# Performance work log

Measured on AMD Instinct MI355X. Metric: run time of the kernel, lower is better.

The kernel has to match this reference:

```python
import jax, jax.numpy as jnp
import numpy as np

N = 4096      # number of projected gaussians
W = 512       # screen width
H = 512       # screen height
TL = 64       # tile_length
NT = W // TL  # tiles per axis (8) -> NT*NT = 64 tiles


def setup_inputs() -> dict:
    key = jax.random.key(0)
    k1, k2, k3, k4, k5 = jax.random.split(key, 5)
    xy = jax.random.uniform(k1, (N, 2), dtype=jnp.float32) * W          # screen positions
    depth = jax.random.uniform(k2, (N, 1), dtype=jnp.float32) * 10.0 + 0.1
    pos2d = jnp.concatenate([xy, depth], axis=1)                        # [N,3] = (x, y, depth)
    A = jax.random.normal(k3, (N, 2, 2), dtype=jnp.float32)
    cov2d = 9.0 * jnp.einsum('nij,nkj->nik', A, A) + jnp.eye(2, dtype=jnp.float32)  # PSD, ~3px sigma
    opacity = jax.random.uniform(k4, (N,), dtype=jnp.float32)
    color = jax.random.uniform(k5, (N, 3), dtype=jnp.float32)           # SH-evaluated RGB (pre +0.5 clamp)
    return {"pos2d": pos2d, "cov2d": cov2d, "opacity": opacity, "color": color}


def _render(pos2d, cov2d, opacity, color):
    # Global depth sort == per-tile argsort of the masked subset (order is preserved).
    order = jnp.argsort(pos2d[:, 2])
    pos = pos2d[order]
    cov = cov2d[order]
    op = opacity[order]
    col = jnp.clip(color[order] + 0.5, 0.0, None)  # color = clamp(eval_sh + 0.5, min=0)

    a, b = cov[:, 0, 0], cov[:, 0, 1]
    c, d = cov[:, 1, 0], cov[:, 1, 1]
    trace = a + d
    det = a * d - b * c
    term2 = 0.5 * jnp.sqrt(jnp.clip(trace * trace - 4.0 * det, 0.0, None))
    radius = 3.0 * jnp.sqrt(jnp.maximum(0.5 * trace - term2, 0.5 * trace + term2))

    inv_det = 1.0 / det
    ia = d * inv_det
    ib = -b * inv_det
    ic = -c * inv_det
    id_ = a * inv_det
    px, py = pos[:, 0], pos[:, 1]

    def tile_fn(tid):
        tx = tid // NT
        ty = tid % NT
        left = (tx * TL).astype(jnp.float32)
        top = (ty * TL).astype(jnp.float32)
        xs = left + jnp.arange(TL, dtype=jnp.float32)  # pixel x coords of tile rows
        ys = top + jnp.arange(TL, dtype=jnp.float32)   # pixel y coords of tile cols
        # gaussian's 3-sigma circle overlaps tile rect -> included in this tile
        inmask = ((px + radius >= left) & (px - radius < left + TL) &
                  (py + radius >= top) & (py - radius < top + TL))
        dx = xs[:, None, None] - px[None, None, :]  # [TL,1,K]
        dy = ys[None, :, None] - py[None, None, :]  # [1,TL,K]
        # mahalanobis distance: d^T Sigma^{-1} d  -> [TL,TL,K]
        q = ia * dx * dx + (ib + ic) * dx * dy + id_ * dy * dy
        prob = jnp.exp(-0.5 * q)
        alpha = jnp.where(inmask, jnp.clip(op * prob, 0.01, 0.99), 0.0)  # excluded -> alpha 0
        # transmittance: cumprod of (1 - alpha) shifted by one (front-to-back)
        ones = jnp.ones((TL, TL, 1), dtype=alpha.dtype)
        weight = jnp.cumprod(jnp.concatenate([ones, 1.0 - alpha[:, :, :-1]], axis=2), axis=2)
        return jnp.einsum('xyk,kc->xyc', alpha * weight, col)  # [TL,TL,3]

    tiles = jax.lax.map(tile_fn, jnp.arange(NT * NT))  # [NT*NT, TL, TL, 3]
    img = tiles.reshape(NT, NT, TL, TL, 3).transpose(0, 2, 1, 3, 4).reshape(W, H, 3)
    return img


def reference(pos2d, cov2d, opacity, color):
    return _render(pos2d, cov2d, opacity, color)
```

## Files before the change

### kernel.cpp

```cpp
#include <hip/hip_runtime.h>


#define N_G    4096
#define W_IMG  512
#define TL_    64
#define NTILES 64
#define LOG2E  1.44269504088896340736f

typedef float v2f __attribute__((ext_vector_type(2)));


__global__ __launch_bounds__(256)
void gs_preprocess(const float* __restrict__ pos2d,
                   const float* __restrict__ cov2d,
                   const float* __restrict__ opacity,
                   const float* __restrict__ color,
                   float4* __restrict__ a4,
                   float4* __restrict__ b4,
                   float* __restrict__ c1,
                   unsigned long long* __restrict__ tmask) {
    __shared__ __align__(16) float s_depth[N_G];
    const int t = threadIdx.x;

    for (int k = t; k < N_G; k += 256)
        s_depth[k] = pos2d[k * 3 + 2];
    __syncthreads();

    const int g = t >> 5;
    const int s = t & 31;
    const int i = blockIdx.x * 8 + g;
    const float di = s_depth[i];

    const float4* s_d4 = (const float4*)s_depth;
    int rank = 0;
    #pragma unroll 8
    for (int k = 0; k < 32; ++k) {
        const int j4 = s + 32 * k;
        const float4 d = s_d4[j4];
        const int j = 4 * j4;
        rank += (d.x < di) || (d.x == di && (j + 0) < i);
        rank += (d.y < di) || (d.y == di && (j + 1) < i);
        rank += (d.z < di) || (d.z == di && (j + 2) < i);
        rank += (d.w < di) || (d.w == di && (j + 3) < i);
    }
    rank += __shfl_xor(rank, 1);
    rank += __shfl_xor(rank, 2);
    rank += __shfl_xor(rank, 4);
    rank += __shfl_xor(rank, 8);
    rank += __shfl_xor(rank, 16);

    if (s == 0) {
        const float px = pos2d[i * 3 + 0];
        const float py = pos2d[i * 3 + 1];
        const float a = cov2d[i * 4 + 0];
        const float b = cov2d[i * 4 + 1];
        const float c = cov2d[i * 4 + 2];
        const float d = cov2d[i * 4 + 3];

        const float trace = a + d;
        const float det = a * d - b * c;
        const float tmp = trace * trace - 4.0f * det;
        const float term2 = 0.5f * sqrtf(fmaxf(tmp, 0.0f));
        const float radius = 3.0f * sqrtf(fmaxf(0.5f * trace - term2, 0.5f * trace + term2));
        const float inv_det = 1.0f / det;
        const float ia  = d * inv_det;
        const float ibc = (-b * inv_det) + (-c * inv_det);
        const float idd = a * inv_det;

        const float op = opacity[i];
        const float cr = fmaxf(color[i * 3 + 0] + 0.5f, 0.0f);
        const float cg = fmaxf(color[i * 3 + 1] + 0.5f, 0.0f);
        const float cb = fmaxf(color[i * 3 + 2] + 0.5f, 0.0f);

        unsigned int xm = 0, ym = 0;
        #pragma unroll
        for (int tc = 0; tc < 8; ++tc) {
            const float lo = (float)(tc * TL_);
            if ((px + radius >= lo) && (px - radius < lo + (float)TL_)) xm |= 1u << tc;
            if ((py + radius >= lo) && (py - radius < lo + (float)TL_)) ym |= 1u << tc;
        }
        unsigned long long m = 0ull;
        #pragma unroll
        for (int tc = 0; tc < 8; ++tc)
            if (xm & (1u << tc)) m |= (unsigned long long)ym << (8 * tc);

        a4[rank] = make_float4(px, py, -0.5f * ia * LOG2E, -0.5f * ibc * LOG2E);
        b4[rank] = make_float4(-0.5f * idd * LOG2E, __log2f(op), cr, cg);
        c1[rank] = cb;
        tmask[rank] = m;
    }
}

__global__ __launch_bounds__(256, 2)
void gs_render(const float4* __restrict__ a4,
               const float4* __restrict__ b4,
               const float* __restrict__ c1,
               const unsigned long long* __restrict__ tmask,
               float* __restrict__ out) {
    __shared__ unsigned short s_list[N_G];
    __shared__ int s_wcnt[4];
    __shared__ __align__(16) float4 s_wa[4][64];
    __shared__ __align__(16) float4 s_wb[4][64];
    __shared__ float s_wc[4][64];
    __shared__ __align__(16) float4 s_m[3][512];

    const int id = blockIdx.x;
    const int sub  = id >> 6;
    const int tile = ((id & 63) * 21 + sub * 11) & 63;
    const int tx = tile >> 3;
    const int ty = tile & 7;
    const int t = threadIdx.x;
    const int wave = t >> 6;
    const int lane = t & 63;

    unsigned int bits = 0;
    int wcnt = 0;
    #pragma unroll 4
    for (int it = 0; it < 16; ++it) {
        const int g = wave * 1024 + it * 64 + lane;
        const bool m = (tmask[g] >> tile) & 1ull;
        bits |= (m ? 1u : 0u) << it;
        wcnt += __popcll(__ballot(m));
    }
    if (lane == 0) s_wcnt[wave] = wcnt;
    __syncthreads();
    const int c0 = s_wcnt[0], c1_ = s_wcnt[1], c2 = s_wcnt[2], c3 = s_wcnt[3];
    const int total = c0 + c1_ + c2 + c3;
    int base = (wave > 0 ? c0 : 0) + (wave > 1 ? c1_ : 0) + (wave > 2 ? c2 : 0);
    #pragma unroll 4
    for (int it = 0; it < 16; ++it) {
        const bool m = (bits >> it) & 1u;
        const unsigned long long bal = __ballot(m);
        const int prefix = __popcll(bal & ((1ULL << lane) - 1ULL));
        if (m) s_list[base + prefix] = (unsigned short)(wave * 1024 + it * 64 + lane);
        base += __popcll(bal);
    }
    __syncthreads();

    const int s0 = (wave * total) >> 2;
    const int s1 = ((wave + 1) * total) >> 2;

    const int X0 = tx * TL_ + sub * 8;
    const int Y  = ty * TL_ + lane;
    const float fY = (float)Y;

    const v2f fX0 = {(float)(X0 + 0), (float)(X0 + 1)};
    const v2f fX1 = {(float)(X0 + 2), (float)(X0 + 3)};
    const v2f fX2 = {(float)(X0 + 4), (float)(X0 + 5)};
    const v2f fX3 = {(float)(X0 + 6), (float)(X0 + 7)};

    v2f R0 = {0.f, 0.f}, R1 = R0, R2 = R0, R3 = R0;
    v2f G0 = R0, G1 = R0, G2 = R0, G3 = R0;
    v2f B0 = R0, B1 = R0, B2 = R0, B3 = R0;
    v2f T0 = {1.f, 1.f}, T1 = T0, T2 = T0, T3 = T0;

    float4* const wa = s_wa[wave];
    float4* const wb = s_wb[wave];
    float*  const wc = s_wc[wave];

    float4 va, vb;
    float vc = 0.f;
    if (s0 + lane < s1) {
        const int g = s_list[s0 + lane];
        va = a4[g]; vb = b4[g]; vc = c1[g];
    }

    for (int c = s0; c < s1; c += 64) {
        const int n = min(64, s1 - c);
        if (lane < n) { wa[lane] = va; wb[lane] = vb; wc[lane] = vc; }
        const int cn = c + 64;
        if (cn + lane < s1) {
            const int g = s_list[cn + lane];
            va = a4[g]; vb = b4[g]; vc = c1[g];
        }
        #pragma unroll 4
        for (int k = 0; k < n; ++k) {
            const float4 A  = wa[k];
            const float4 Bv = wb[k];
            const float cbv = wc[k];

            const float dy   = fY - A.y;
            const float qbdy = A.w * dy;
            const float bse  = Bv.x * dy * dy + Bv.y;
            const v2f az2 = {A.z, A.z};
            const v2f ax2 = {A.x, A.x};
            const v2f qb2 = {qbdy, qbdy};
            const v2f bs2 = {bse, bse};
            const v2f lo2 = {0.01f, 0.01f};
            const v2f hi2 = {0.99f, 0.99f};
            const v2f cr2 = {Bv.z, Bv.z};
            const v2f cg2 = {Bv.w, Bv.w};
            const v2f cb2 = {cbv, cbv};
#define PX_PAIR(FXP, Tp, Rp, Gp, Bp)                                          \
            {                                                                 \
                const v2f dx = FXP - ax2;                                     \
                v2f q = __builtin_elementwise_fma(az2, dx, qb2);              \
                q = __builtin_elementwise_fma(q, dx, bs2);                    \
                v2f e;                                                        \
                e.x = exp2f(q.x); e.y = exp2f(q.y);                           \
                v2f al;                                                       \
                al.x = __builtin_amdgcn_fmed3f(e.x, lo2.x, hi2.x);            \
                al.y = __builtin_amdgcn_fmed3f(e.y, lo2.y, hi2.y);            \
                const v2f w_ = al * Tp;                                       \
                Rp = __builtin_elementwise_fma(w_, cr2, Rp);                  \
                Gp = __builtin_elementwise_fma(w_, cg2, Gp);                  \
                Bp = __builtin_elementwise_fma(w_, cb2, Bp);                  \
                Tp = Tp - w_;                                                 \
            }
            PX_PAIR(fX0, T0, R0, G0, B0)
            PX_PAIR(fX1, T1, R1, G1, B1)
            PX_PAIR(fX2, T2, R2, G2, B2)
            PX_PAIR(fX3, T3, R3, G3, B3)
#undef PX_PAIR
        }
    }

    if (wave != 0) {
        float4* const m = s_m[wave - 1];
#define PUB(j, Tp, Rp, Gp, Bp)                                                \
        m[(2*j + 0) * 64 + lane] = make_float4(Rp.x, Gp.x, Bp.x, Tp.x);       \
        m[(2*j + 1) * 64 + lane] = make_float4(Rp.y, Gp.y, Bp.y, Tp.y);
        PUB(0, T0, R0, G0, B0)
        PUB(1, T1, R1, G1, B1)
        PUB(2, T2, R2, G2, B2)
        PUB(3, T3, R3, G3, B3)
#undef PUB
    }
    __syncthreads();
    if (wave == 0) {
#define OUT_PX(i, tv, rv, gv, bv)                                             \
        {                                                                     \
            const int p = (i) * 64 + lane;                                    \
            const float4 m1 = s_m[0][p];                                      \
            const float4 m2 = s_m[1][p];                                      \
            const float4 m3 = s_m[2][p];                                      \
            float r = m2.x + m2.w * m3.x;                                     \
            float g = m2.y + m2.w * m3.y;                                     \
            float b = m2.z + m2.w * m3.z;                                     \
            r = m1.x + m1.w * r;                                              \
            g = m1.y + m1.w * g;                                              \
            b = m1.z + m1.w * b;                                              \
            const int o = ((X0 + (i)) * W_IMG + Y) * 3;                       \
            out[o + 0] = rv + tv * r;                                         \
            out[o + 1] = gv + tv * g;                                         \
            out[o + 2] = bv + tv * b;                                         \
        }
        OUT_PX(0, T0.x, R0.x, G0.x, B0.x)
        OUT_PX(1, T0.y, R0.y, G0.y, B0.y)
        OUT_PX(2, T1.x, R1.x, G1.x, B1.x)
        OUT_PX(3, T1.y, R1.y, G1.y, B1.y)
        OUT_PX(4, T2.x, R2.x, G2.x, B2.x)
        OUT_PX(5, T2.y, R2.y, G2.y, B2.y)
        OUT_PX(6, T3.x, R3.x, G3.x, B3.x)
        OUT_PX(7, T3.y, R3.y, G3.y, B3.y)
#undef OUT_PX
    }
}

extern "C" void kernel_launch(void* const* d_in, const int* in_sizes, int n_in,
                              void* d_out, int out_size, void* d_ws, size_t ws_size,
                              hipStream_t stream) {
    const float* pos2d   = (const float*)d_in[0];
    const float* cov2d   = (const float*)d_in[1];
    const float* opacity = (const float*)d_in[2];
    const float* color   = (const float*)d_in[3];
    float* out = (float*)d_out;

    char* ws = (char*)d_ws;
    float4* a4 = (float4*)(ws);
    float4* b4 = (float4*)(ws + 65536);
    float*  c1 = (float*)(ws + 131072);
    unsigned long long* tm = (unsigned long long*)(ws + 147456);

    gs_preprocess<<<N_G / 8, 256, 0, stream>>>(pos2d, cov2d, opacity, color,
                                               a4, b4, c1, tm);
    gs_render<<<NTILES * 8, 256, 0, stream>>>(a4, b4, c1, tm, out);
}
```

Baseline: 33.99 us.

## Split render depth range across eight waves with tree-reduced compositing

Doubles the render block from 4 to 8 waves. Each wave takes one eighth of the depth-sorted gaussian list for its tile slice, so the serial per-wave compositing chain gets shorter. Partial (RGB, transmittance) results are then merged front-to-back in a three-level pairwise tree through shared memory, replacing the single-wave three-way merge. This adds more barriers and shared memory use, and launch bounds of 512 threads with 4 blocks requested may squeeze registers.

```diff
diff --git a/kernel.cpp b/kernel.cpp
--- a/kernel.cpp
+++ b/kernel.cpp
@@ -91,18 +91,18 @@
     }
 }
 
-__global__ __launch_bounds__(256, 2)
+__global__ __launch_bounds__(512, 4)
 void gs_render(const float4* __restrict__ a4,
                const float4* __restrict__ b4,
                const float* __restrict__ c1,
                const unsigned long long* __restrict__ tmask,
                float* __restrict__ out) {
     __shared__ unsigned short s_list[N_G];
-    __shared__ int s_wcnt[4];
-    __shared__ __align__(16) float4 s_wa[4][64];
-    __shared__ __align__(16) float4 s_wb[4][64];
-    __shared__ float s_wc[4][64];
-    __shared__ __align__(16) float4 s_m[3][512];
+    __shared__ int s_wcnt[8];
+    __shared__ __align__(16) float4 s_wa[8][64];
+    __shared__ __align__(16) float4 s_wb[8][64];
+    __shared__ float s_wc[8][64];
+    __shared__ __align__(16) float4 s_m[4][512];
 
     const int id = blockIdx.x;
     const int sub  = id >> 6;
@@ -116,29 +116,33 @@
     unsigned int bits = 0;
     int wcnt = 0;
     #pragma unroll 4
-    for (int it = 0; it < 16; ++it) {
-        const int g = wave * 1024 + it * 64 + lane;
+    for (int it = 0; it < 8; ++it) {
+        const int g = wave * 512 + it * 64 + lane;
         const bool m = (tmask[g] >> tile) & 1ull;
         bits |= (m ? 1u : 0u) << it;
         wcnt += __popcll(__ballot(m));
     }
     if (lane == 0) s_wcnt[wave] = wcnt;
     __syncthreads();
-    const int c0 = s_wcnt[0], c1_ = s_wcnt[1], c2 = s_wcnt[2], c3 = s_wcnt[3];
-    const int total = c0 + c1_ + c2 + c3;
-    int base = (wave > 0 ? c0 : 0) + (wave > 1 ? c1_ : 0) + (wave > 2 ? c2 : 0);
+    int total = 0, base = 0;
+    #pragma unroll
+    for (int w = 0; w < 8; ++w) {
+        const int c = s_wcnt[w];
+        total += c;
+        if (w < wave) base += c;
+    }
     #pragma unroll 4
-    for (int it = 0; it < 16; ++it) {
+    for (int it = 0; it < 8; ++it) {
         const bool m = (bits >> it) & 1u;
         const unsigned long long bal = __ballot(m);
         const int prefix = __popcll(bal & ((1ULL << lane) - 1ULL));
-        if (m) s_list[base + prefix] = (unsigned short)(wave * 1024 + it * 64 + lane);
+        if (m) s_list[base + prefix] = (unsigned short)(wave * 512 + it * 64 + lane);
         base += __popcll(bal);
     }
     __syncthreads();
 
-    const int s0 = (wave * total) >> 2;
-    const int s1 = ((wave + 1) * total) >> 2;
+    const int s0 = (wave * total) >> 3;
+    const int s1 = ((wave + 1) * total) >> 3;
 
     const int X0 = tx * TL_ + sub * 8;
     const int Y  = ty * TL_ + lane;
@@ -215,35 +219,56 @@
         }
     }
 
-    if (wave != 0) {
-        float4* const m = s_m[wave - 1];
-#define PUB(j, Tp, Rp, Gp, Bp)                                                \
-        m[(2*j + 0) * 64 + lane] = make_float4(Rp.x, Gp.x, Bp.x, Tp.x);       \
-        m[(2*j + 1) * 64 + lane] = make_float4(Rp.y, Gp.y, Bp.y, Tp.y);
-        PUB(0, T0, R0, G0, B0)
-        PUB(1, T1, R1, G1, B1)
-        PUB(2, T2, R2, G2, B2)
-        PUB(3, T3, R3, G3, B3)
-#undef PUB
-    }
+#define PUBLISH(buf)                                                          \
+    {                                                                         \
+        (buf)[0 * 64 + lane] = make_float4(R0.x, G0.x, B0.x, T0.x);           \
+        (buf)[1 * 64 + lane] = make_float4(R0.y, G0.y, B0.y, T0.y);           \
+        (buf)[2 * 64 + lane] = make_float4(R1.x, G1.x, B1.x, T1.x);           \
+        (buf)[3 * 64 + lane] = make_float4(R1.y, G1.y, B1.y, T1.y);           \
+        (buf)[4 * 64 + lane] = make_float4(R2.x, G2.x, B2.x, T2.x);           \
+        (buf)[5 * 64 + lane] = make_float4(R2.y, G2.y, B2.y, T2.y);           \
+        (buf)[6 * 64 + lane] = make_float4(R3.x, G3.x, B3.x, T3.x);           \
+        (buf)[7 * 64 + lane] = make_float4(R3.y, G3.y, B3.y, T3.y);           \
+    }
+#define COMPOSE(buf)                                                          \
+    {                                                                         \
+        _Pragma("unroll")                                                     \
+        for (int j = 0; j < 4; ++j) {                                         \
+            const float4 m0 = (buf)[(2 * j + 0) * 64 + lane];                 \
+            const float4 m1 = (buf)[(2 * j + 1) * 64 + lane];                 \
+            const v2f mr = {m0.x, m1.x};                                      \
+            const v2f mg = {m0.y, m1.y};                                      \
+            const v2f mb = {m0.z, m1.z};                                      \
+            const v2f mt = {m0.w, m1.w};                                      \
+            v2f* Rj = j == 0 ? &R0 : j == 1 ? &R1 : j == 2 ? &R2 : &R3;       \
+            v2f* Gj = j == 0 ? &G0 : j == 1 ? &G1 : j == 2 ? &G2 : &G3;       \
+            v2f* Bj = j == 0 ? &B0 : j == 1 ? &B1 : j == 2 ? &B2 : &B3;       \
+            v2f* Tj = j == 0 ? &T0 : j == 1 ? &T1 : j == 2 ? &T2 : &T3;       \
+            *Rj = __builtin_elementwise_fma(*Tj, mr, *Rj);                    \
+            *Gj = __builtin_elementwise_fma(*Tj, mg, *Gj);                    \
+            *Bj = __builtin_elementwise_fma(*Tj, mb, *Bj);                    \
+            *Tj = *Tj * mt;                                                   \
+        }                                                                     \
+    }
+
+    if (wave & 1) PUBLISH(s_m[wave >> 1]);
+    __syncthreads();
+    if (!(wave & 1)) COMPOSE(s_m[wave >> 1]);
+    if (wave == 2) PUBLISH(s_m[1]);
+    if (wave == 6) PUBLISH(s_m[3]);
+    __syncthreads();
+    if (wave == 0) COMPOSE(s_m[1]);
+    if (wave == 4) COMPOSE(s_m[3]);
+    if (wave == 4) PUBLISH(s_m[3]);
     __syncthreads();
     if (wave == 0) {
+        COMPOSE(s_m[3]);
 #define OUT_PX(i, tv, rv, gv, bv)                                             \
         {                                                                     \
-            const int p = (i) * 64 + lane;                                    \
-            const float4 m1 = s_m[0][p];                                      \
-            const float4 m2 = s_m[1][p];                                      \
-            const float4 m3 = s_m[2][p];                                      \
-            float r = m2.x + m2.w * m3.x;                                     \
-            float g = m2.y + m2.w * m3.y;                                     \
-            float b = m2.z + m2.w * m3.z;                                     \
-            r = m1.x + m1.w * r;                                              \
-            g = m1.y + m1.w * g;                                              \
-            b = m1.z + m1.w * b;                                              \
             const int o = ((X0 + (i)) * W_IMG + Y) * 3;                       \
-            out[o + 0] = rv + tv * r;                                         \
-            out[o + 1] = gv + tv * g;                                         \
-            out[o + 2] = bv + tv * b;                                         \
+            out[o + 0] = rv;                                                  \
+            out[o + 1] = gv;                                                  \
+            out[o + 2] = bv;                                                  \
         }
         OUT_PX(0, T0.x, R0.x, G0.x, B0.x)
         OUT_PX(1, T0.y, R0.y, G0.y, B0.y)
@@ -255,6 +280,8 @@
         OUT_PX(7, T3.y, R3.y, G3.y, B3.y)
 #undef OUT_PX
     }
+#undef PUBLISH
+#undef COMPOSE
 }
 
 extern "C" void kernel_launch(void* const* d_in, const int* in_sizes, int n_in,
@@ -274,5 +301,5 @@
 
     gs_preprocess<<<N_G / 8, 256, 0, stream>>>(pos2d, cov2d, opacity, color,
                                                a4, b4, c1, tm);
-    gs_render<<<NTILES * 8, 256, 0, stream>>>(a4, b4, c1, tm, out);
+    gs_render<<<NTILES * 8, 512, 0, stream>>>(a4, b4, c1, tm, out);
 }
```

Result: no change. 33.59 us (-1.2%).
